# Kernel optimization log

Measured on AMD Instinct MI355X. Metric: run time of the kernel, lower is better.

The kernel has to match this reference:

```python
import jax, jax.numpy as jnp
import numpy as np

NEG_SLOPE = 0.01  # torch leaky_relu default

def leaky_relu(x):
    return jnp.where(x >= 0, x, NEG_SLOPE * x)

def setup_inputs() -> dict:
    key = jax.random.key(0)
    k1, k2, k3, k4, k5, k6 = jax.random.split(key, 6)
    B, N, D, E = 4, 20000, 128, 100000
    s = 1.0 / np.sqrt(D)
    embeddings = jax.random.normal(k1, (B, N, D), dtype=jnp.float32)
    edges_ij = jax.random.randint(k2, (E, 2), 0, N, dtype=jnp.int64)
    W6 = jax.random.uniform(k3, (D, D), jnp.float32, -s, s)   # theta6 (in,out)
    W7 = jax.random.uniform(k4, (D, D), jnp.float32, -s, s)   # theta7 (in,out)
    w5 = jax.random.uniform(k5, (3 * D,), jnp.float32, -1.0 / np.sqrt(3 * D), 1.0 / np.sqrt(3 * D))  # theta5
    w_noop = jax.random.uniform(k6, (D,), jnp.float32, -s, s)  # noop
    return {"embeddings": embeddings, "edges_ij": edges_ij, "W6": W6, "W7": W7, "w5": w5, "w_noop": w_noop}

def reference(embeddings, edges_ij, W6, W7, w5, w_noop):
    B, N, D = embeddings.shape
    u = edges_ij[:, 0]
    v = edges_ij[:, 1]
    g = embeddings.sum(axis=1)                      # [B,D] (normalize=False)
    g_proj = g @ W6                                  # [B,D]
    node_proj = jnp.einsum('bnd,de->bne', embeddings, W7)  # [B,N,D]
    # theta5(leaky_relu(cat[g,i,j])) == lrelu(g)@w5_g + lrelu(i)@w5_i + lrelu(j)@w5_j
    # (leaky_relu is elementwise, theta5 has no bias), so project per-node THEN
    # gather scalars per edge — avoids the [B,E,3D] concat intermediate.
    w5_g, w5_i, w5_j = w5[:D], w5[D:2 * D], w5[2 * D:]
    qg = leaky_relu(g_proj) @ w5_g                   # [B]
    qi = leaky_relu(node_proj) @ w5_i                # [B,N]
    qj = leaky_relu(node_proj) @ w5_j                # [B,N]
    edge_q = qg[:, None] + qi[:, u] + qj[:, v]       # [B,E]
    noop_q = (g @ w_noop)[:, None]                   # [B,1]
    return jnp.concatenate([edge_q, noop_q], axis=1)  # [B,E+1]
```

## Files before the change

### kernel.cpp

```cpp
#include <hip/hip_runtime.h>
#include <hip/hip_bf16.h>

#define B_ 4
#define N_ 20000
#define D_ 128
#define E_ 100000
#define NT_ 1250
#define GX_ 313

typedef __attribute__((ext_vector_type(8))) short bf16x8;
typedef __attribute__((ext_vector_type(4))) float f32x4;


__global__ __launch_bounds__(256) void k_prep(
    const float* __restrict__ W7, const unsigned* __restrict__ ew,
    int* __restrict__ flag, float* __restrict__ g, bf16x8* __restrict__ w7f)
{
    const int bx = blockIdx.x, t = threadIdx.x;
    if (bx == 8) {
        g[t] = 0.f; g[t + 256] = 0.f;
        if (t < 64) {
            unsigned v = ew[2 * t + 1];
            unsigned long long any = __ballot(v != 0u);
            if (t == 0) *flag = (any == 0ULL) ? 1 : 0;
        }
        return;
    }
    int f = bx * 256 + t;
    int tt = f >> 8, s = (f >> 6) & 3, lane = f & 63;
    int kg = lane >> 4, rc = lane & 15;
    int col = tt * 16 + rc, k0 = s * 32 + kg * 8;
    union { bf16x8 v; __hip_bfloat16 h[8]; } pk;
    #pragma unroll
    for (int m = 0; m < 8; ++m)
        pk.h[m] = __float2bfloat16(W7[(k0 + m) * D_ + col]);
    w7f[f] = pk.v;
}

__global__ __launch_bounds__(256) void k_main(
    const float* __restrict__ emb, const bf16x8* __restrict__ w7f,
    const float* __restrict__ w5, float* __restrict__ gpart,
    float* __restrict__ qi, float* __restrict__ qj)
{
    __shared__ bf16x8 sB[2048];

    const int t = threadIdx.x, b = blockIdx.y;
    const int wv = t >> 6, lane = t & 63, rc = lane & 15, kg = lane >> 4;
    const int tile = blockIdx.x * 4 + wv;
    const int tc = (tile < NT_) ? tile : (NT_ - 1);

    const float4* p = (const float4*)(emb + (size_t)b * N_ * D_)
                      + ((size_t)(tc * 16 + rc)) * 32 + kg * 2;
    float4 a[8];
    #pragma unroll
    for (int s = 0; s < 4; ++s) { a[2*s] = p[s*8]; a[2*s+1] = p[s*8+1]; }

    {
        const uint4* src = (const uint4*)w7f;
        uint4* dst = (uint4*)sB;
        #pragma unroll
        for (int i = 0; i < 8; ++i) dst[t + 256 * i] = src[t + 256 * i];
    }
    __syncthreads();

    bf16x8 pk[4];
    #pragma unroll
    for (int s = 0; s < 4; ++s) {
        union { bf16x8 v; __hip_bfloat16 h[8]; } u;
        float4 x = a[2*s], y = a[2*s+1];
        u.h[0] = __float2bfloat16(x.x); u.h[1] = __float2bfloat16(x.y);
        u.h[2] = __float2bfloat16(x.z); u.h[3] = __float2bfloat16(x.w);
        u.h[4] = __float2bfloat16(y.x); u.h[5] = __float2bfloat16(y.y);
        u.h[6] = __float2bfloat16(y.z); u.h[7] = __float2bfloat16(y.w);
        pk[s] = u.v;
    }

    f32x4 acc[8] = {};
    #pragma unroll
    for (int s = 0; s < 4; ++s) {
        #pragma unroll
        for (int tt = 0; tt < 8; ++tt) {
            bf16x8 bb = sB[tt * 256 + s * 64 + lane];
            acc[tt] = __builtin_amdgcn_mfma_f32_16x16x32_bf16(pk[s], bb, acc[tt], 0, 0, 0);
        }
    }

    float qip[4] = {0,0,0,0}, qjp[4] = {0,0,0,0};
    #pragma unroll
    for (int tt = 0; tt < 8; ++tt) {
        int col = tt * 16 + rc;
        float wi = w5[D_ + col], wj = w5[2 * D_ + col];
        #pragma unroll
        for (int r = 0; r < 4; ++r) {
            float pv = acc[tt][r];
            float lr = (pv >= 0.f) ? pv : 0.01f * pv;
            qip[r] += lr * wi; qjp[r] += lr * wj;
        }
    }
    #pragma unroll
    for (int m = 1; m < 16; m <<= 1) {
        #pragma unroll
        for (int r = 0; r < 4; ++r) {
            qip[r] += __shfl_xor(qip[r], m);
            qjp[r] += __shfl_xor(qjp[r], m);
        }
    }
    if (tile < NT_ && rc == 0) {
        #pragma unroll
        for (int r = 0; r < 4; ++r) {
            int node = tile * 16 + kg * 4 + r;
            qi[b * N_ + node] = qip[r];
            qj[b * N_ + node] = qjp[r];
        }
    }

    #pragma unroll
    for (int m = 1; m < 16; m <<= 1) {
        #pragma unroll
        for (int i = 0; i < 8; ++i) {
            a[i].x += __shfl_xor(a[i].x, m);
            a[i].y += __shfl_xor(a[i].y, m);
            a[i].z += __shfl_xor(a[i].z, m);
            a[i].w += __shfl_xor(a[i].w, m);
        }
    }
    if (tile < NT_ && rc == 0) {
        float* gp = gpart + (size_t)tile * 512 + b * 128;
        #pragma unroll
        for (int s = 0; s < 4; ++s) {
            int c0 = s * 32 + kg * 8;
            *reinterpret_cast<float4*>(gp + c0)     = a[2*s];
            *reinterpret_cast<float4*>(gp + c0 + 4) = a[2*s+1];
        }
    }
}

__global__ __launch_bounds__(512) void k_greduce(
    const float* __restrict__ gpart, float* __restrict__ g)
{
    const int t = threadIdx.x;
    const int c0 = blockIdx.x * 25;
    float s = 0.f;
    #pragma unroll 5
    for (int i = 0; i < 25; ++i)
        s += gpart[(size_t)(c0 + i) * 512 + t];
    atomicAdd(&g[t], s);
}

__global__ __launch_bounds__(256) void k_qg(
    const float* __restrict__ g, const float* __restrict__ W6,
    const float* __restrict__ w5, const float* __restrict__ wno,
    float* __restrict__ qg, float* __restrict__ out)
{
    __shared__ float sg[128];
    __shared__ float sp2[2][128];
    __shared__ float sr[2], srn[2];
    const int b = blockIdx.x, t = threadIdx.x;
    const int col = t & 127, h = t >> 7;

    if (t < 128) sg[t] = g[b * D_ + t];
    __syncthreads();

    float pv = 0.f;
    #pragma unroll 8
    for (int d = h * 64; d < h * 64 + 64; ++d)
        pv += sg[d] * W6[d * D_ + col];
    sp2[h][col] = pv;
    __syncthreads();

    if (t < 128) {
        float pp = sp2[0][t] + sp2[1][t];
        float lr = (pp >= 0.f) ? pp : 0.01f * pp;
        float vq = lr * w5[t];
        float vn = sg[t] * wno[t];
        #pragma unroll
        for (int m = 1; m < 64; m <<= 1) {
            vq += __shfl_xor(vq, m);
            vn += __shfl_xor(vn, m);
        }
        if ((t & 63) == 0) { sr[t >> 6] = vq; srn[t >> 6] = vn; }
    }
    __syncthreads();
    if (t == 0) {
        qg[b] = sr[0] + sr[1];
        out[(size_t)b * (E_ + 1) + E_] = srn[0] + srn[1];
    }
}

__global__ __launch_bounds__(256) void k_edge(
    const int* __restrict__ edges, const int* __restrict__ flag,
    const float* __restrict__ qg, const float* __restrict__ qi,
    const float* __restrict__ qj, float* __restrict__ out)
{
    int e = blockIdx.x * 256 + threadIdx.x;
    if (e >= E_) return;
    int u, v;
    if (*flag) { int4 w = ((const int4*)edges)[e]; u = w.x; v = w.z; }
    else       { int2 w = ((const int2*)edges)[e]; u = w.x; v = w.y; }
    float q0 = qg[0], q1 = qg[1], q2 = qg[2], q3 = qg[3];
    out[0 * (size_t)(E_ + 1) + e] = q0 + qi[0 * N_ + u] + qj[0 * N_ + v];
    out[1 * (size_t)(E_ + 1) + e] = q1 + qi[1 * N_ + u] + qj[1 * N_ + v];
    out[2 * (size_t)(E_ + 1) + e] = q2 + qi[2 * N_ + u] + qj[2 * N_ + v];
    out[3 * (size_t)(E_ + 1) + e] = q3 + qi[3 * N_ + u] + qj[3 * N_ + v];
}

extern "C" void kernel_launch(void* const* d_in, const int* in_sizes, int n_in,
                              void* d_out, int out_size, void* d_ws, size_t ws_size,
                              hipStream_t stream)
{
    const float* emb   = (const float*)d_in[0];
    const int*   edges = (const int*)d_in[1];
    const float* W6    = (const float*)d_in[2];
    const float* W7    = (const float*)d_in[3];
    const float* w5    = (const float*)d_in[4];
    const float* wno   = (const float*)d_in[5];
    float* out = (float*)d_out;

    float* W = (float*)d_ws;
    int*    flag  = (int*)W;
    float*  qg    = W + 8;
    float*  g     = W + 128;
    bf16x8* w7f   = (bf16x8*)(W + 1024);
    float*  gpart = W + 9216;
    float*  qi    = W + 649216;
    float*  qj    = W + 729216;

    hipLaunchKernelGGL(k_prep, dim3(9), dim3(256), 0, stream,
                       W7, (const unsigned*)edges, flag, g, w7f);
    hipLaunchKernelGGL(k_main, dim3(GX_, B_), dim3(256), 0, stream,
                       emb, w7f, w5, gpart, qi, qj);
    hipLaunchKernelGGL(k_greduce, dim3(50), dim3(512), 0, stream, gpart, g);
    hipLaunchKernelGGL(k_qg, dim3(B_), dim3(256), 0, stream,
                       g, W6, w5, wno, qg, out);
    hipLaunchKernelGGL(k_edge, dim3((E_ + 255) / 256), dim3(256), 0, stream,
                       edges, flag, qg, qi, qj, out);
}
```

Before: 39.35 us.

## Load W7 fragments directly into registers and fuse g-reduction with qg via last-block

k_main no longer stages the bf16 W7 fragments through shared memory with a barrier. Each wave loads its 32 fragments straight from global/L2 into registers, and interleaved w5 weights are precomputed in k_prep. The g partial reduction is now done before the MFMA work. k_qg is merged into k_greduce using an atomic counter so the last block computes qg and the noop output, which removes one kernel launch. The trade-offs are much higher register pressure in k_main (128 extra VGPRs for B fragments), redundant global loads of W7 per wave, and a serial tail in the last reduction block.

```diff
diff --git a/kernel.cpp b/kernel.cpp
--- a/kernel.cpp
+++ b/kernel.cpp
@@ -7,18 +7,23 @@
 #define E_ 100000
 #define NT_ 1250
 #define GX_ 313
+#define GRB_ 50
 
 typedef __attribute__((ext_vector_type(8))) short bf16x8;
 typedef __attribute__((ext_vector_type(4))) float f32x4;
 
 
 __global__ __launch_bounds__(256) void k_prep(
-    const float* __restrict__ W7, const unsigned* __restrict__ ew,
-    int* __restrict__ flag, float* __restrict__ g, bf16x8* __restrict__ w7f)
+    const float* __restrict__ W7, const float* __restrict__ w5,
+    const unsigned* __restrict__ ew, int* __restrict__ flag,
+    unsigned* __restrict__ cnt, float* __restrict__ g,
+    float2* __restrict__ w5f, bf16x8* __restrict__ w7f)
 {
     const int bx = blockIdx.x, t = threadIdx.x;
     if (bx == 8) {
         g[t] = 0.f; g[t + 256] = 0.f;
+        if (t < 128) w5f[t] = make_float2(w5[D_ + t], w5[2 * D_ + t]);
+        if (t == 0) *cnt = 0u;
         if (t < 64) {
             unsigned v = ew[2 * t + 1];
             unsigned long long any = __ballot(v != 0u);
@@ -39,11 +44,9 @@
 
 __global__ __launch_bounds__(256) void k_main(
     const float* __restrict__ emb, const bf16x8* __restrict__ w7f,
-    const float* __restrict__ w5, float* __restrict__ gpart,
+    const float2* __restrict__ w5f, float* __restrict__ gpart,
     float* __restrict__ qi, float* __restrict__ qj)
 {
-    __shared__ bf16x8 sB[2048];
-
     const int t = threadIdx.x, b = blockIdx.y;
     const int wv = t >> 6, lane = t & 63, rc = lane & 15, kg = lane >> 4;
     const int tile = blockIdx.x * 4 + wv;
@@ -55,13 +58,16 @@
     #pragma unroll
     for (int s = 0; s < 4; ++s) { a[2*s] = p[s*8]; a[2*s+1] = p[s*8+1]; }
 
-    {
-        const uint4* src = (const uint4*)w7f;
-        uint4* dst = (uint4*)sB;
-        #pragma unroll
-        for (int i = 0; i < 8; ++i) dst[t + 256 * i] = src[t + 256 * i];
-    }
-    __syncthreads();
+    bf16x8 bf[4][8];
+    #pragma unroll
+    for (int s = 0; s < 4; ++s)
+        #pragma unroll
+        for (int tt = 0; tt < 8; ++tt)
+            bf[s][tt] = w7f[tt * 256 + s * 64 + lane];
+
+    float2 wij[8];
+    #pragma unroll
+    for (int tt = 0; tt < 8; ++tt) wij[tt] = w5f[tt * 16 + rc];
 
     bf16x8 pk[4];
     #pragma unroll
@@ -75,45 +81,6 @@
         pk[s] = u.v;
     }
 
-    f32x4 acc[8] = {};
-    #pragma unroll
-    for (int s = 0; s < 4; ++s) {
-        #pragma unroll
-        for (int tt = 0; tt < 8; ++tt) {
-            bf16x8 bb = sB[tt * 256 + s * 64 + lane];
-            acc[tt] = __builtin_amdgcn_mfma_f32_16x16x32_bf16(pk[s], bb, acc[tt], 0, 0, 0);
-        }
-    }
-
-    float qip[4] = {0,0,0,0}, qjp[4] = {0,0,0,0};
-    #pragma unroll
-    for (int tt = 0; tt < 8; ++tt) {
-        int col = tt * 16 + rc;
-        float wi = w5[D_ + col], wj = w5[2 * D_ + col];
-        #pragma unroll
-        for (int r = 0; r < 4; ++r) {
-            float pv = acc[tt][r];
-            float lr = (pv >= 0.f) ? pv : 0.01f * pv;
-            qip[r] += lr * wi; qjp[r] += lr * wj;
-        }
-    }
-    #pragma unroll
-    for (int m = 1; m < 16; m <<= 1) {
-        #pragma unroll
-        for (int r = 0; r < 4; ++r) {
-            qip[r] += __shfl_xor(qip[r], m);
-            qjp[r] += __shfl_xor(qjp[r], m);
-        }
-    }
-    if (tile < NT_ && rc == 0) {
-        #pragma unroll
-        for (int r = 0; r < 4; ++r) {
-            int node = tile * 16 + kg * 4 + r;
-            qi[b * N_ + node] = qip[r];
-            qj[b * N_ + node] = qjp[r];
-        }
-    }
-
     #pragma unroll
     for (int m = 1; m < 16; m <<= 1) {
         #pragma unroll
@@ -133,57 +100,113 @@
             *reinterpret_cast<float4*>(gp + c0 + 4) = a[2*s+1];
         }
     }
+
+    f32x4 acc[8] = {};
+    #pragma unroll
+    for (int s = 0; s < 4; ++s)
+        #pragma unroll
+        for (int tt = 0; tt < 8; ++tt)
+            acc[tt] = __builtin_amdgcn_mfma_f32_16x16x32_bf16(pk[s], bf[s][tt], acc[tt], 0, 0, 0);
+
+    float qip[4] = {0,0,0,0}, qjp[4] = {0,0,0,0};
+    #pragma unroll
+    for (int tt = 0; tt < 8; ++tt) {
+        #pragma unroll
+        for (int r = 0; r < 4; ++r) {
+            float pv = acc[tt][r];
+            float lr = (pv >= 0.f) ? pv : 0.01f * pv;
+            qip[r] += lr * wij[tt].x;
+            qjp[r] += lr * wij[tt].y;
+        }
+    }
+    #pragma unroll
+    for (int m = 1; m < 16; m <<= 1) {
+        #pragma unroll
+        for (int r = 0; r < 4; ++r) {
+            qip[r] += __shfl_xor(qip[r], m);
+            qjp[r] += __shfl_xor(qjp[r], m);
+        }
+    }
+    if (tile < NT_ && rc == 0) {
+        #pragma unroll
+        for (int r = 0; r < 4; ++r) {
+            int node = tile * 16 + kg * 4 + r;
+            qi[b * N_ + node] = qip[r];
+            qj[b * N_ + node] = qjp[r];
+        }
+    }
 }
 
 __global__ __launch_bounds__(512) void k_greduce(
-    const float* __restrict__ gpart, float* __restrict__ g)
-{
-    const int t = threadIdx.x;
-    const int c0 = blockIdx.x * 25;
-    float s = 0.f;
-    #pragma unroll 5
-    for (int i = 0; i < 25; ++i)
-        s += gpart[(size_t)(c0 + i) * 512 + t];
-    atomicAdd(&g[t], s);
-}
-
-__global__ __launch_bounds__(256) void k_qg(
-    const float* __restrict__ g, const float* __restrict__ W6,
+    const float* __restrict__ gpart, float* __restrict__ g,
+    unsigned* __restrict__ cnt, const float* __restrict__ W6,
     const float* __restrict__ w5, const float* __restrict__ wno,
     float* __restrict__ qg, float* __restrict__ out)
 {
-    __shared__ float sg[128];
-    __shared__ float sp2[2][128];
-    __shared__ float sr[2], srn[2];
-    const int b = blockIdx.x, t = threadIdx.x;
-    const int col = t & 127, h = t >> 7;
-
-    if (t < 128) sg[t] = g[b * D_ + t];
-    __syncthreads();
-
-    float pv = 0.f;
-    #pragma unroll 8
-    for (int d = h * 64; d < h * 64 + 64; ++d)
-        pv += sg[d] * W6[d * D_ + col];
-    sp2[h][col] = pv;
-    __syncthreads();
-
+    __shared__ float sp[4][B_][D_];
+    __shared__ float sr[2][B_], srn[2][B_];
+    __shared__ int lastf;
+
+    const int t = threadIdx.x;
+    {
+        const int c0 = blockIdx.x * 25;
+        float s = 0.f;
+        #pragma unroll 5
+        for (int i = 0; i < 25; ++i)
+            s += gpart[(size_t)(c0 + i) * 512 + t];
+        atomicAdd(&g[t], s);
+    }
+    __threadfence();
+    __syncthreads();
+    if (t == 0) {
+        unsigned old = atomicAdd(cnt, 1u);
+        lastf = (old == GRB_ - 1) ? 1 : 0;
+    }
+    __syncthreads();
+    if (!lastf) return;
+    __threadfence();
+
+    const int col = t & 127, q = t >> 7;
+    {
+        float p[B_] = {0, 0, 0, 0};
+        for (int d = q * 32; d < q * 32 + 32; ++d) {
+            float w6 = W6[d * D_ + col];
+            #pragma unroll
+            for (int b = 0; b < B_; ++b) p[b] += g[b * D_ + d] * w6;
+        }
+        #pragma unroll
+        for (int b = 0; b < B_; ++b) sp[q][b][col] = p[b];
+    }
+    __syncthreads();
     if (t < 128) {
-        float pp = sp2[0][t] + sp2[1][t];
-        float lr = (pp >= 0.f) ? pp : 0.01f * pp;
-        float vq = lr * w5[t];
-        float vn = sg[t] * wno[t];
+        float vq[B_], vn[B_];
+        #pragma unroll
+        for (int b = 0; b < B_; ++b) {
+            float pp = sp[0][b][t] + sp[1][b][t] + sp[2][b][t] + sp[3][b][t];
+            float lr = (pp >= 0.f) ? pp : 0.01f * pp;
+            vq[b] = lr * w5[t];
+            vn[b] = g[b * D_ + t] * wno[t];
+        }
         #pragma unroll
         for (int m = 1; m < 64; m <<= 1) {
-            vq += __shfl_xor(vq, m);
-            vn += __shfl_xor(vn, m);
-        }
-        if ((t & 63) == 0) { sr[t >> 6] = vq; srn[t >> 6] = vn; }
+            #pragma unroll
+            for (int b = 0; b < B_; ++b) {
+                vq[b] += __shfl_xor(vq[b], m);
+                vn[b] += __shfl_xor(vn[b], m);
+            }
+        }
+        if ((t & 63) == 0) {
+            #pragma unroll
+            for (int b = 0; b < B_; ++b) { sr[t >> 6][b] = vq[b]; srn[t >> 6][b] = vn[b]; }
+        }
     }
     __syncthreads();
     if (t == 0) {
-        qg[b] = sr[0] + sr[1];
-        out[(size_t)b * (E_ + 1) + E_] = srn[0] + srn[1];
+        #pragma unroll
+        for (int b = 0; b < B_; ++b) {
+            qg[b] = sr[0][b] + sr[1][b];
+            out[(size_t)b * (E_ + 1) + E_] = srn[0][b] + srn[1][b];
+        }
     }
 }
 
@@ -217,21 +240,22 @@
     float* out = (float*)d_out;
 
     float* W = (float*)d_ws;
-    int*    flag  = (int*)W;
-    float*  qg    = W + 8;
-    float*  g     = W + 128;
-    bf16x8* w7f   = (bf16x8*)(W + 1024);
-    float*  gpart = W + 9216;
-    float*  qi    = W + 649216;
-    float*  qj    = W + 729216;
+    int*      flag  = (int*)W;
+    unsigned* cnt   = (unsigned*)(W + 4);
+    float*    qg    = W + 8;
+    float*    g     = W + 128;
+    float2*   w5f   = (float2*)(W + 640);
+    bf16x8*   w7f   = (bf16x8*)(W + 1024);
+    float*    gpart = W + 9216;
+    float*    qi    = W + 649216;
+    float*    qj    = W + 729216;
 
     hipLaunchKernelGGL(k_prep, dim3(9), dim3(256), 0, stream,
-                       W7, (const unsigned*)edges, flag, g, w7f);
+                       W7, w5, (const unsigned*)edges, flag, cnt, g, w5f, w7f);
     hipLaunchKernelGGL(k_main, dim3(GX_, B_), dim3(256), 0, stream,
-                       emb, w7f, w5, gpart, qi, qj);
-    hipLaunchKernelGGL(k_greduce, dim3(50), dim3(512), 0, stream, gpart, g);
-    hipLaunchKernelGGL(k_qg, dim3(B_), dim3(256), 0, stream,
-                       g, W6, w5, wno, qg, out);
+                       emb, w7f, w5f, gpart, qi, qj);
+    hipLaunchKernelGGL(k_greduce, dim3(GRB_), dim3(512), 0, stream,
+                       gpart, g, cnt, W6, w5, wno, qg, out);
     hipLaunchKernelGGL(k_edge, dim3((E_ + 255) / 256), dim3(256), 0, stream,
                        edges, flag, qg, qi, qj, out);
 }
```

Result: slower. 55.77 us (+41.7%).
